# Kernel optimization log

Hardware: AMD Instinct MI355X
Metric: run time of the kernel (lower is better)

## Reference

```python
import jax, jax.numpy as jnp
import numpy as np

N = 50000      # nodes
E = 800000     # edges (before self-loops)
IN = 256       # in_channels
HID = 16       # hidden_channels per head
HEADS = 8
OUT = 64       # out_channels (classes)
NEG_SLOPE = 0.2  # PyG GATConv leaky_relu slope


def setup_inputs() -> dict:
    key = jax.random.key(0)
    ks = jax.random.split(key, 10)
    x = jax.random.normal(ks[0], (N, IN), jnp.float32)
    edge_index = jax.random.randint(ks[1], (2, E), 0, N, dtype=jnp.int32)
    g = lambda k, shape: jax.random.normal(k, shape, jnp.float32) * (1.0 / np.sqrt(shape[0]))
    W1 = g(ks[2], (IN, HEADS * HID))
    a_src1 = jax.random.normal(ks[3], (HEADS, HID), jnp.float32) * 0.1
    a_dst1 = jax.random.normal(ks[4], (HEADS, HID), jnp.float32) * 0.1
    b1 = jnp.zeros((HEADS * HID,), jnp.float32)
    W2 = g(ks[5], (HEADS * HID, OUT))
    a_src2 = jax.random.normal(ks[6], (1, OUT), jnp.float32) * 0.1
    a_dst2 = jax.random.normal(ks[7], (1, OUT), jnp.float32) * 0.1
    b2 = jnp.zeros((OUT,), jnp.float32)
    return {"x": x, "edge_index": edge_index, "W1": W1, "a_src1": a_src1,
            "a_dst1": a_dst1, "b1": b1, "W2": W2, "a_src2": a_src2,
            "a_dst2": a_dst2, "b2": b2}


def gat_conv(x, src, dst, W, a_s, a_d, b, heads, concat):
    # x: [n, f]; edges src->dst; attention softmax over incoming edges of dst
    n = x.shape[0]
    h = (x @ W).reshape(n, heads, -1)                 # [n, H, d]
    al_s = jnp.einsum('nhd,hd->nh', h, a_s)           # [n, H]
    al_d = jnp.einsum('nhd,hd->nh', h, a_d)
    e = jax.nn.leaky_relu(al_s[src] + al_d[dst], negative_slope=NEG_SLOPE)  # [E, H]
    m = jax.ops.segment_max(e, dst, num_segments=n)   # stable scatter-softmax
    ex = jnp.exp(e - m[dst])
    den = jax.ops.segment_sum(ex, dst, num_segments=n)
    alpha = ex / (den[dst] + 1e-16)                   # [E, H]
    out = jax.ops.segment_sum(h[src] * alpha[:, :, None], dst, num_segments=n)  # [n, H, d]
    out = out.reshape(n, -1) if concat else out.mean(axis=1)
    return out + b


def reference(x, edge_index, W1, a_src1, a_dst1, b1, W2, a_src2, a_dst2, b2):
    # inference mode: dropout disabled. PyG GATConv adds self-loops by default.
    n = x.shape[0]
    loop = jnp.arange(n, dtype=edge_index.dtype)
    ei = jnp.concatenate([edge_index, jnp.stack([loop, loop])], axis=1)
    src, dst = ei[0], ei[1]
    h = gat_conv(x, src, dst, W1, a_src1, a_dst1, b1, HEADS, True)
    h = jax.nn.elu(h)
    h = gat_conv(h, src, dst, W2, a_src2, a_dst2, b2, 1, False)
    return jax.nn.log_softmax(h, axis=1)
```

## Files before the change

kernel.cpp:

```cpp
#include <hip/hip_runtime.h>
#include <hip/hip_bf16.h>


typedef __attribute__((ext_vector_type(8))) short short8;
typedef __attribute__((ext_vector_type(4))) float f4;
typedef __attribute__((ext_vector_type(2))) float float2v;

#define NCHUNK 64
#define NRANGE 4
#define RSIZE 16384
#define CONVB 80

#define A1PAD 72
#define B1PAD 264
#define G2PAD 136

__device__ __forceinline__ unsigned short f2bf(float f) {
  unsigned int u = __builtin_bit_cast(unsigned int, f);
  u += 0x7fffu + ((u >> 16) & 1u);
  return (unsigned short)(u >> 16);
}
__device__ __forceinline__ float bf2f(unsigned short h) {
  unsigned int u = ((unsigned int)h) << 16;
  return __builtin_bit_cast(float, u);
}

__device__ __forceinline__ unsigned char f2fp8(float f) {
  unsigned int u = __builtin_bit_cast(unsigned int, f);
  unsigned int s = (u >> 24) & 0x80u;
  float a = fabsf(f);
  a = fminf(a, 448.f);
  if (a < 0.015625f) {
    int m = (int)rintf(a * 512.f);
    return (unsigned char)(s | (unsigned)m);
  }
  unsigned int ub = __builtin_bit_cast(unsigned int, a);
  ub += 0xFFFFFu + ((ub >> 20) & 1u);
  unsigned int e = (ub >> 23) - 120u;
  unsigned int m = (ub >> 20) & 7u;
  if (e > 15u) { e = 15u; m = 6u; }
  return (unsigned char)(s | (e << 3) | m);
}

__global__ __launch_bounds__(512) void hist_kernel(const int* __restrict__ ei,
                                                   int* __restrict__ hist,
                                                   const float* __restrict__ W1,
                                                   const float* __restrict__ W2,
                                                   unsigned short* __restrict__ Wt1,
                                                   unsigned short* __restrict__ Wt2,
                                                   int E, int N, int ET, int CS) {
  if (blockIdx.x >= NCHUNK * NRANGE) {
    int i = (blockIdx.x - NCHUNK * NRANGE) * 512 + threadIdx.x;
    if (i < 128 * 256) {
      int n = i >> 8, k = i & 255;
      Wt1[i] = f2bf(W1[k * 128 + n]);
    } else {
      int j = i - 128 * 256;
      if (j < 64 * 128) {
        int n = j >> 7, k = j & 127;
        Wt2[j] = f2bf(W2[k * 64 + n]);
      }
    }
    return;
  }
  __shared__ int lh[RSIZE];
  const int c = blockIdx.x & (NCHUNK - 1);
  const int r = blockIdx.x >> 6;
  const int base = r * RSIZE;
  for (int i = threadIdx.x; i < RSIZE; i += 512) lh[i] = 0;
  __syncthreads();
  const int e0 = c * CS, e1 = min(e0 + CS, ET);
  for (int e = e0 + threadIdx.x; e < e1; e += 512) {
    int d = (e < E) ? ei[E + e] : (e - E);
    unsigned dl = (unsigned)(d - base);
    if (dl < RSIZE) atomicAdd(&lh[dl], 1);
  }
  __syncthreads();
  for (int i = threadIdx.x; i < RSIZE; i += 512) {
    int d = base + i;
    if (d < N) hist[c * N + d] = lh[i];
  }
}

__global__ __launch_bounds__(256) void colscan_kernel(int* __restrict__ hist,
                                                      int* __restrict__ deg, int N) {
  int d = blockIdx.x * 256 + threadIdx.x;
  if (d >= N) return;
  int run = 0;
#pragma unroll 8
  for (int c = 0; c < NCHUNK; ++c) {
    int v = hist[c * N + d];
    hist[c * N + d] = run;
    run += v;
  }
  deg[d] = run;
}

__global__ __launch_bounds__(1024) void scan1_kernel(const int* __restrict__ deg,
                                                     int* __restrict__ rowptr,
                                                     int* __restrict__ bsum, int N) {
  __shared__ int wtot[16];
  const int lane = threadIdx.x & 63, wid = threadIdx.x >> 6;
  int i = blockIdx.x * 1024 + threadIdx.x;
  int v = (i < N) ? deg[i] : 0;
  int incl = v;
#pragma unroll
  for (int off = 1; off < 64; off <<= 1) {
    int t = __shfl_up(incl, off, 64);
    if (lane >= off) incl += t;
  }
  if (lane == 63) wtot[wid] = incl;
  __syncthreads();
  int woff = 0;
#pragma unroll
  for (int w = 0; w < 16; ++w) woff += (w < wid) ? wtot[w] : 0;
  if (i < N) rowptr[i] = woff + incl - v;
  if (threadIdx.x == 1023) bsum[blockIdx.x] = woff + incl;
}

__global__ __launch_bounds__(256) void scan3_kernel(int* __restrict__ rowptr,
                                                    const int* __restrict__ bsum,
                                                    int N, int ET) {
  int lane = threadIdx.x & 63;
  int g = blockIdx.x >> 2;
  int bv = (lane < g) ? bsum[lane] : 0;
#pragma unroll
  for (int off = 32; off; off >>= 1) bv += __shfl_xor(bv, off, 64);
  int i = blockIdx.x * 256 + threadIdx.x;
  if (i < N) rowptr[i] += bv;
  if (i == N) rowptr[N] = ET;
}

__global__ __launch_bounds__(512) void scatter2_kernel(const int* __restrict__ ei,
                                                       const int* __restrict__ hist,
                                                       const int* __restrict__ rowptr,
                                                       int* __restrict__ csr_src,
                                                       int E, int N, int ET, int CS) {
  __shared__ int lh[RSIZE];
  const int c = blockIdx.x & (NCHUNK - 1);
  const int r = blockIdx.x >> 6;
  const int base = r * RSIZE;
  for (int i = threadIdx.x; i < RSIZE; i += 512) {
    int d = base + i;
    lh[i] = (d < N) ? (rowptr[d] + hist[c * N + d]) : 0;
  }
  __syncthreads();
  const int e0 = c * CS, e1 = min(e0 + CS, ET);
  for (int e = e0 + threadIdx.x; e < e1; e += 512) {
    int s, d;
    if (e < E) { s = ei[e]; d = ei[E + e]; }
    else       { s = e - E; d = s; }
    unsigned dl = (unsigned)(d - base);
    if (dl < RSIZE) {
      int slot = atomicAdd(&lh[dl], 1);
      csr_src[slot] = s;
    }
  }
}

__global__ __launch_bounds__(256) void gemm1_mfma(const float* __restrict__ X,
                                                  const unsigned short* __restrict__ Wt,
                                                  const float* __restrict__ as1,
                                                  const float* __restrict__ ad1,
                                                  unsigned char* __restrict__ H,
                                                  float* __restrict__ als,
                                                  float* __restrict__ ald,
                                                  int M) {
  __shared__ unsigned short Bs[64 * B1PAD];
  __shared__ unsigned short As[2][64 * A1PAD];
  const int t = threadIdx.x;
  const int ln = t & 63;
  const int wv = t >> 6;
  const int ml = ln & 15, q = ln >> 4;
  const int ch = blockIdx.x & 1;
  const int rb = (blockIdx.x >> 1) * 64;
  const int r0 = rb + wv * 16;
  const int alr = wv * 16 + ml;

  int srow[4], skg[4];
#pragma unroll
  for (int i = 0; i < 4; ++i) {
    int g = i * 256 + t;
    srow[i] = g >> 4;
    skg[i] = g & 15;
  }

  float4 astg[4];
#pragma unroll
  for (int i = 0; i < 4; ++i)
    astg[i] = *(const float4*)(X + (size_t)min(rb + srow[i], M - 1) * 256 + skg[i] * 4);

#pragma unroll
  for (int i = 0; i < 8; ++i) {
    int g = i * 256 + t;
    int brow = g >> 5, bc = g & 31;
    *(short8*)&Bs[brow * B1PAD + bc * 8] =
        *(const short8*)(Wt + (size_t)(ch * 64 + brow) * 256 + bc * 8);
  }

#pragma unroll
  for (int i = 0; i < 4; ++i) {
    ushort4 pk;
    pk.x = f2bf(astg[i].x); pk.y = f2bf(astg[i].y);
    pk.z = f2bf(astg[i].z); pk.w = f2bf(astg[i].w);
    *(ushort4*)&As[0][srow[i] * A1PAD + skg[i] * 4] = pk;
  }
  __syncthreads();

  f4 acc[4];
#pragma unroll
  for (int b = 0; b < 4; ++b) acc[b] = (f4)0.f;

#pragma unroll
  for (int s = 0; s < 4; ++s) {
    const int buf = s & 1;
    if (s < 3) {
#pragma unroll
      for (int i = 0; i < 4; ++i)
        astg[i] = *(const float4*)(X + (size_t)min(rb + srow[i], M - 1) * 256 +
                                   (s + 1) * 64 + skg[i] * 4);
    }
#pragma unroll
    for (int kk = 0; kk < 2; ++kk) {
      short8 av = *(const short8*)&As[buf][alr * A1PAD + kk * 32 + q * 8];
#pragma unroll
      for (int b = 0; b < 4; ++b) {
        short8 bfr = *(const short8*)&Bs[(b * 16 + ml) * B1PAD + s * 64 + kk * 32 + q * 8];
        acc[b] = __builtin_amdgcn_mfma_f32_16x16x32_bf16(av, bfr, acc[b], 0, 0, 0);
      }
    }
    if (s < 3) {
#pragma unroll
      for (int i = 0; i < 4; ++i) {
        ushort4 pk;
        pk.x = f2bf(astg[i].x); pk.y = f2bf(astg[i].y);
        pk.z = f2bf(astg[i].z); pk.w = f2bf(astg[i].w);
        *(ushort4*)&As[buf ^ 1][srow[i] * A1PAD + skg[i] * 4] = pk;
      }
    }
    __syncthreads();
  }

#pragma unroll
  for (int i = 0; i < 4; ++i) {
    int rr = r0 + q * 4 + i;
    bool ok = rr < M;
    if (ok) {
#pragma unroll
      for (int b = 0; b < 4; ++b)
        H[(size_t)rr * 128 + ch * 64 + b * 16 + ml] = f2fp8(acc[b][i]);
    }
#pragma unroll
    for (int b = 0; b < 4; ++b) {
      float ps = acc[b][i] * as1[ch * 64 + b * 16 + ml];
      float pd = acc[b][i] * ad1[ch * 64 + b * 16 + ml];
#pragma unroll
      for (int off = 1; off < 16; off <<= 1) {
        ps += __shfl_xor(ps, off, 16);
        pd += __shfl_xor(pd, off, 16);
      }
      if (ok && ml == b) {
        als[(size_t)rr * 8 + ch * 4 + b] = ps;
        ald[(size_t)rr * 8 + ch * 4 + b] = pd;
      }
    }
  }
}

__global__ __launch_bounds__(256) void gemm2_mfma(const unsigned short* __restrict__ Xb,
                                                  const unsigned short* __restrict__ Wt,
                                                  const float* __restrict__ as2,
                                                  const float* __restrict__ ad2,
                                                  unsigned char* __restrict__ H,
                                                  float* __restrict__ als,
                                                  float* __restrict__ ald,
                                                  int M) {
  __shared__ unsigned short Asl[64 * G2PAD];
  __shared__ unsigned short Bsl[64 * G2PAD];
  const int t = threadIdx.x;
  const int ln = t & 63;
  const int wv = t >> 6;
  const int ml = ln & 15, q = ln >> 4;
  const int rb = blockIdx.x * 64;
  const int r0 = rb + wv * 16;
  const int alr = wv * 16 + ml;

#pragma unroll
  for (int i = 0; i < 4; ++i) {
    int g = i * 256 + t;
    int row = g >> 4, kg = g & 15;
    *(short8*)&Asl[row * G2PAD + kg * 8] =
        *(const short8*)(Xb + (size_t)min(rb + row, M - 1) * 128 + kg * 8);
    *(short8*)&Bsl[row * G2PAD + kg * 8] =
        *(const short8*)(Wt + (size_t)row * 128 + kg * 8);
  }
  __syncthreads();

  short8 av[4];
#pragma unroll
  for (int s = 0; s < 4; ++s)
    av[s] = *(const short8*)&Asl[alr * G2PAD + s * 32 + q * 8];

  f4 acc[4];
#pragma unroll
  for (int b = 0; b < 4; ++b) acc[b] = (f4)0.f;

#pragma unroll
  for (int s = 0; s < 4; ++s) {
#pragma unroll
    for (int b = 0; b < 4; ++b) {
      short8 bfr = *(const short8*)&Bsl[(b * 16 + ml) * G2PAD + s * 32 + q * 8];
      acc[b] = __builtin_amdgcn_mfma_f32_16x16x32_bf16(av[s], bfr, acc[b], 0, 0, 0);
    }
  }

#pragma unroll
  for (int i = 0; i < 4; ++i) {
    int rr = r0 + q * 4 + i;
    bool ok = rr < M;
    if (ok) {
#pragma unroll
      for (int b = 0; b < 4; ++b)
        H[(size_t)rr * 64 + b * 16 + ml] = f2fp8(acc[b][i]);
    }
    float ps = 0.f, pd = 0.f;
#pragma unroll
    for (int b = 0; b < 4; ++b) {
      ps += acc[b][i] * as2[b * 16 + ml];
      pd += acc[b][i] * ad2[b * 16 + ml];
    }
#pragma unroll
    for (int off = 1; off < 16; off <<= 1) {
      ps += __shfl_xor(ps, off, 16);
      pd += __shfl_xor(pd, off, 16);
    }
    if (ok && ml == 0) { als[rr] = ps; ald[rr] = pd; }
  }
}

__global__ __launch_bounds__(256) void attn1_kernel(
    const unsigned char* __restrict__ h1, const float* __restrict__ als,
    const float* __restrict__ ald, const float* __restrict__ b1,
    const int* __restrict__ rowptr, const int* __restrict__ csr_src,
    unsigned short* __restrict__ helu, int N) {
  int d = __builtin_amdgcn_readfirstlane(
      (blockIdx.x * blockDim.x + threadIdx.x) >> 6);
  int lane = threadIdx.x & 63;
  if (d >= N) return;
  const int hh = lane >> 3;
  const int hw = lane & 7;
  const int ew = lane >> 3;
  const float aldp = ald[d * 8 + hw];
  const int beg = rowptr[d], end = rowptr[d + 1];
  const unsigned char* h1l = h1 + 2 * lane;
  float den = 0.f, ax = 0.f, ay = 0.f;

  int idx0 = beg + ew;
  int se = csr_src[idx0 < end ? idx0 : end - 1];
  for (int p0 = beg; p0 < end; p0 += 8) {
    int p1 = p0 + 8;
    int se_n = se;
    if (p1 < end) {
      int idx1 = p1 + ew;
      se_n = csr_src[idx1 < end ? idx1 : end - 1];
    }
    float v = als[se * 8 + hw] + aldp;
    v = fmaxf(v, 0.2f * v);
    float w = ((p0 + ew) < end) ? __expf(v) : 0.f;
    int sjv[8];
#pragma unroll
    for (int j = 0; j < 8; ++j) sjv[j] = __shfl(se, j * 8);
    unsigned short pkv[8];
#pragma unroll
    for (int j = 0; j < 8; ++j)
      pkv[j] = *(const unsigned short*)(h1l + (size_t)sjv[j] * 128);
#pragma unroll
    for (int j = 0; j < 8; ++j) {
      float wj = __shfl(w, j * 8 + hh);
      float2v g = __builtin_amdgcn_cvt_pk_f32_fp8(pkv[j], false);
      den += wj; ax += wj * g.x; ay += wj * g.y;
    }
    se = se_n;
  }

  float inv = 1.0f / (den + 1e-16f);
  float2 bb = *(const float2*)(b1 + 2 * lane);
  float o0 = ax * inv + bb.x;
  float o1 = ay * inv + bb.y;
  o0 = o0 > 0.f ? o0 : __expf(o0) - 1.0f;
  o1 = o1 > 0.f ? o1 : __expf(o1) - 1.0f;
  ushort2 ov; ov.x = f2bf(o0); ov.y = f2bf(o1);
  *(ushort2*)(helu + (size_t)d * 128 + 2 * lane) = ov;
}

__global__ __launch_bounds__(256) void attn2_kernel(
    const unsigned char* __restrict__ h2, const float* __restrict__ als,
    const float* __restrict__ ald, const float* __restrict__ b2,
    const int* __restrict__ rowptr, const int* __restrict__ csr_src,
    float* __restrict__ out, int N) {
  int d = __builtin_amdgcn_readfirstlane(
      (blockIdx.x * blockDim.x + threadIdx.x) >> 6);
  int lane = threadIdx.x & 63;
  if (d >= N) return;
  const float aldd = ald[d];
  const int beg = rowptr[d], end = rowptr[d + 1];
  const unsigned char* h2l = h2 + lane;
  float den = 0.f, acc = 0.f;

  int idx0 = beg + lane;
  int se = csr_src[idx0 < end ? idx0 : end - 1];
  for (int p0 = beg; p0 < end; p0 += 64) {
    int p1 = p0 + 64;
    int se_n = se;
    if (p1 < end) {
      int i1 = p1 + lane;
      se_n = csr_src[i1 < end ? i1 : end - 1];
    }
    float v = als[se] + aldd;
    v = fmaxf(v, 0.2f * v);
    float w = ((p0 + lane) < end) ? __expf(v) : 0.f;
    int cnt = min(64, end - p0);
    for (int j0 = 0; j0 < cnt; j0 += 8) {
      int sjv[8];
#pragma unroll
      for (int j = 0; j < 8; ++j) sjv[j] = __shfl(se, j0 + j);
      float gv[8];
#pragma unroll
      for (int j = 0; j < 8; ++j)
        gv[j] = __builtin_amdgcn_cvt_f32_fp8(h2l[(size_t)sjv[j] * 64], 0);
#pragma unroll
      for (int j = 0; j < 8; ++j) {
        float wj = __shfl(w, j0 + j);
        den += wj; acc += wj * gv[j];
      }
    }
    se = se_n;
  }

  float z = acc / (den + 1e-16f) + b2[lane];
  float zm = z;
#pragma unroll
  for (int off = 32; off; off >>= 1) zm = fmaxf(zm, __shfl_xor(zm, off, 64));
  float ex = __expf(z - zm), se2 = ex;
#pragma unroll
  for (int off = 32; off; off >>= 1) se2 += __shfl_xor(se2, off, 64);
  out[(size_t)d * 64 + lane] = z - zm - __logf(se2);
}

extern "C" void kernel_launch(void* const* d_in, const int* in_sizes, int n_in,
                              void* d_out, int out_size, void* d_ws, size_t ws_size,
                              hipStream_t stream) {
  const int N = in_sizes[0] / 256;
  const int E = in_sizes[1] / 2;
  const int ET = E + N;
  const int CS = (ET + NCHUNK - 1) / NCHUNK;
  const int NB = (N + 1023) / 1024;

  const float* x   = (const float*)d_in[0];
  const int*   ei  = (const int*)d_in[1];
  const float* W1  = (const float*)d_in[2];
  const float* as1 = (const float*)d_in[3];
  const float* ad1 = (const float*)d_in[4];
  const float* b1  = (const float*)d_in[5];
  const float* W2  = (const float*)d_in[6];
  const float* as2 = (const float*)d_in[7];
  const float* ad2 = (const float*)d_in[8];
  const float* b2  = (const float*)d_in[9];
  float* out = (float*)d_out;

  char* p = (char*)d_ws;
  unsigned char* h1f8 = (unsigned char*)p; p += (size_t)N * 128;
  unsigned char* h2f8 = h1f8;
  unsigned short* helu = (unsigned short*)p; p += (size_t)NCHUNK * N * 4;
  int* hist = (int*)helu;
  unsigned short* Wt1  = (unsigned short*)p; p += (size_t)128 * 256 * 2;
  unsigned short* Wt2  = (unsigned short*)p; p += (size_t)64 * 128 * 2;
  float* als1 = (float*)p; p += (size_t)N * 8 * 4;
  float* ald1 = (float*)p; p += (size_t)N * 8 * 4;
  float* als2 = (float*)p; p += (size_t)N * 4;
  float* ald2 = (float*)p; p += (size_t)N * 4;
  int* deg     = (int*)p; p += (size_t)N * 4;
  int* rowptr  = (int*)p; p += (size_t)(N + 1) * 4;
  int* bsum    = (int*)p; p += 64 * 4;
  int* csr_src = (int*)p; p += (size_t)ET * 4;

  hist_kernel<<<NCHUNK * NRANGE + CONVB, 512, 0, stream>>>(ei, hist, W1, W2, Wt1, Wt2,
                                                           E, N, ET, CS);
  colscan_kernel<<<(N + 255) / 256, 256, 0, stream>>>(hist, deg, N);
  scan1_kernel<<<NB, 1024, 0, stream>>>(deg, rowptr, bsum, N);
  scan3_kernel<<<(N + 256) / 256, 256, 0, stream>>>(rowptr, bsum, N, ET);
  scatter2_kernel<<<NCHUNK * NRANGE, 512, 0, stream>>>(ei, hist, rowptr, csr_src, E, N, ET, CS);

  gemm1_mfma<<<2 * ((N + 63) / 64), 256, 0, stream>>>(x, Wt1, as1, ad1, h1f8, als1, ald1, N);
  attn1_kernel<<<(N + 3) / 4, 256, 0, stream>>>(h1f8, als1, ald1, b1, rowptr, csr_src, helu, N);

  gemm2_mfma<<<(N + 63) / 64, 256, 0, stream>>>(helu, Wt2, as2, ad2, h2f8, als2, ald2, N);
  attn2_kernel<<<(N + 3) / 4, 256, 0, stream>>>(h2f8, als2, ald2, b2, rowptr, csr_src, out, N);
}
```

Baseline: 247.6 us.

## Vectorize attention gathers with 16-byte loads and cross-lane reductions

Both attention kernels are remapped so each lane loads a 16-byte chunk of an fp8 source row and accumulates 16 features. Several edges are handled in parallel across lane groups, and partial sums are combined at the end with xor-shuffle reductions. The first layer uses 8 lanes per edge (one per head); the second uses 4 lanes per edge with 16 edges per step. This replaces many narrow per-lane byte and short gathers, plus the per-edge broadcast shuffles, with fewer wide loads. The cost is more registers and a reduction tail of many shuffles per node, which matters at low average degree.

Measured after the change: 282.5 us. +14.1%, slower.

```diff
diff --git a/kernel.cpp b/kernel.cpp
--- a/kernel.cpp
+++ b/kernel.cpp
@@ -347,50 +347,66 @@
       (blockIdx.x * blockDim.x + threadIdx.x) >> 6);
   int lane = threadIdx.x & 63;
   if (d >= N) return;
-  const int hh = lane >> 3;
-  const int hw = lane & 7;
-  const int ew = lane >> 3;
-  const float aldp = ald[d * 8 + hw];
+  const int g = lane >> 3;
+  const int f = lane & 7;
+  const float aldp = ald[d * 8 + f];
   const int beg = rowptr[d], end = rowptr[d + 1];
-  const unsigned char* h1l = h1 + 2 * lane;
-  float den = 0.f, ax = 0.f, ay = 0.f;
-
-  int idx0 = beg + ew;
+  float den = 0.f;
+  float acc[16];
+#pragma unroll
+  for (int k = 0; k < 16; ++k) acc[k] = 0.f;
+
+  int idx0 = beg + g;
   int se = csr_src[idx0 < end ? idx0 : end - 1];
   for (int p0 = beg; p0 < end; p0 += 8) {
     int p1 = p0 + 8;
     int se_n = se;
     if (p1 < end) {
-      int idx1 = p1 + ew;
-      se_n = csr_src[idx1 < end ? idx1 : end - 1];
-    }
-    float v = als[se * 8 + hw] + aldp;
+      int i1 = p1 + g;
+      se_n = csr_src[i1 < end ? i1 : end - 1];
+    }
+    float v = als[se * 8 + f] + aldp;
     v = fmaxf(v, 0.2f * v);
-    float w = ((p0 + ew) < end) ? __expf(v) : 0.f;
-    int sjv[8];
-#pragma unroll
-    for (int j = 0; j < 8; ++j) sjv[j] = __shfl(se, j * 8);
-    unsigned short pkv[8];
-#pragma unroll
-    for (int j = 0; j < 8; ++j)
-      pkv[j] = *(const unsigned short*)(h1l + (size_t)sjv[j] * 128);
+    float w = ((p0 + g) < end) ? __expf(v) : 0.f;
+    short8 hv = *(const short8*)(h1 + (size_t)se * 128 + f * 16);
+    den += w;
 #pragma unroll
     for (int j = 0; j < 8; ++j) {
-      float wj = __shfl(w, j * 8 + hh);
-      float2v g = __builtin_amdgcn_cvt_pk_f32_fp8(pkv[j], false);
-      den += wj; ax += wj * g.x; ay += wj * g.y;
+      float2v u = __builtin_amdgcn_cvt_pk_f32_fp8((unsigned short)hv[j], false);
+      acc[2 * j]     += w * u.x;
+      acc[2 * j + 1] += w * u.y;
     }
     se = se_n;
   }
 
+#pragma unroll
+  for (int off = 8; off < 64; off <<= 1) {
+    den += __shfl_xor(den, off, 64);
+#pragma unroll
+    for (int k = 0; k < 16; ++k) acc[k] += __shfl_xor(acc[k], off, 64);
+  }
+
   float inv = 1.0f / (den + 1e-16f);
-  float2 bb = *(const float2*)(b1 + 2 * lane);
-  float o0 = ax * inv + bb.x;
-  float o1 = ay * inv + bb.y;
-  o0 = o0 > 0.f ? o0 : __expf(o0) - 1.0f;
-  o1 = o1 > 0.f ? o1 : __expf(o1) - 1.0f;
-  ushort2 ov; ov.x = f2bf(o0); ov.y = f2bf(o1);
-  *(ushort2*)(helu + (size_t)d * 128 + 2 * lane) = ov;
+  const float4* bv = (const float4*)(b1 + f * 16);
+  float o[16];
+#pragma unroll
+  for (int qq = 0; qq < 4; ++qq) {
+    float4 bb = bv[qq];
+    o[qq * 4 + 0] = acc[qq * 4 + 0] * inv + bb.x;
+    o[qq * 4 + 1] = acc[qq * 4 + 1] * inv + bb.y;
+    o[qq * 4 + 2] = acc[qq * 4 + 2] * inv + bb.z;
+    o[qq * 4 + 3] = acc[qq * 4 + 3] * inv + bb.w;
+  }
+#pragma unroll
+  for (int k = 0; k < 16; ++k)
+    o[k] = o[k] > 0.f ? o[k] : __expf(o[k]) - 1.0f;
+
+  if (g < 2) {
+    short8 ov;
+#pragma unroll
+    for (int j = 0; j < 8; ++j) ov[j] = (short)f2bf(o[g * 8 + j]);
+    *(short8*)(helu + (size_t)d * 128 + f * 16 + g * 8) = ov;
+  }
 }
 
 __global__ __launch_bounds__(256) void attn2_kernel(
@@ -402,10 +418,14 @@
       (blockIdx.x * blockDim.x + threadIdx.x) >> 6);
   int lane = threadIdx.x & 63;
   if (d >= N) return;
+  const int g = lane >> 2;
+  const int c = lane & 3;
   const float aldd = ald[d];
   const int beg = rowptr[d], end = rowptr[d + 1];
-  const unsigned char* h2l = h2 + lane;
-  float den = 0.f, acc = 0.f;
+  float den = 0.f;
+  float acc[16];
+#pragma unroll
+  for (int k = 0; k < 16; ++k) acc[k] = 0.f;
 
   int idx0 = beg + lane;
   int se = csr_src[idx0 < end ? idx0 : end - 1];
@@ -420,31 +440,59 @@
     v = fmaxf(v, 0.2f * v);
     float w = ((p0 + lane) < end) ? __expf(v) : 0.f;
     int cnt = min(64, end - p0);
-    for (int j0 = 0; j0 < cnt; j0 += 8) {
-      int sjv[8];
-#pragma unroll
-      for (int j = 0; j < 8; ++j) sjv[j] = __shfl(se, j0 + j);
-      float gv[8];
-#pragma unroll
-      for (int j = 0; j < 8; ++j)
-        gv[j] = __builtin_amdgcn_cvt_f32_fp8(h2l[(size_t)sjv[j] * 64], 0);
+    for (int j0 = 0; j0 < cnt; j0 += 16) {
+      int se16 = __shfl(se, j0 + g);
+      float w16 = __shfl(w, j0 + g);
+      short8 hv = *(const short8*)(h2 + (size_t)se16 * 64 + c * 16);
+      den += w16;
 #pragma unroll
       for (int j = 0; j < 8; ++j) {
-        float wj = __shfl(w, j0 + j);
-        den += wj; acc += wj * gv[j];
+        float2v u = __builtin_amdgcn_cvt_pk_f32_fp8((unsigned short)hv[j], false);
+        acc[2 * j]     += w16 * u.x;
+        acc[2 * j + 1] += w16 * u.y;
       }
     }
     se = se_n;
   }
 
-  float z = acc / (den + 1e-16f) + b2[lane];
-  float zm = z;
-#pragma unroll
-  for (int off = 32; off; off >>= 1) zm = fmaxf(zm, __shfl_xor(zm, off, 64));
-  float ex = __expf(z - zm), se2 = ex;
-#pragma unroll
-  for (int off = 32; off; off >>= 1) se2 += __shfl_xor(se2, off, 64);
-  out[(size_t)d * 64 + lane] = z - zm - __logf(se2);
+#pragma unroll
+  for (int off = 4; off < 64; off <<= 1) {
+    den += __shfl_xor(den, off, 64);
+#pragma unroll
+    for (int k = 0; k < 16; ++k) acc[k] += __shfl_xor(acc[k], off, 64);
+  }
+
+  float inv = 1.0f / (den + 1e-16f);
+  const float4* bv = (const float4*)(b2 + c * 16);
+  float z[16];
+#pragma unroll
+  for (int qq = 0; qq < 4; ++qq) {
+    float4 bb = bv[qq];
+    z[qq * 4 + 0] = acc[qq * 4 + 0] * inv + bb.x;
+    z[qq * 4 + 1] = acc[qq * 4 + 1] * inv + bb.y;
+    z[qq * 4 + 2] = acc[qq * 4 + 2] * inv + bb.z;
+    z[qq * 4 + 3] = acc[qq * 4 + 3] * inv + bb.w;
+  }
+  float zm = z[0];
+#pragma unroll
+  for (int k = 1; k < 16; ++k) zm = fmaxf(zm, z[k]);
+  zm = fmaxf(zm, __shfl_xor(zm, 1, 64));
+  zm = fmaxf(zm, __shfl_xor(zm, 2, 64));
+  float se2 = 0.f;
+#pragma unroll
+  for (int k = 0; k < 16; ++k) se2 += __expf(z[k] - zm);
+  se2 += __shfl_xor(se2, 1, 64);
+  se2 += __shfl_xor(se2, 2, 64);
+  float lse = __logf(se2);
+
+  if (lane < 16) {
+    float4 ov;
+    ov.x = z[g * 4 + 0] - zm - lse;
+    ov.y = z[g * 4 + 1] - zm - lse;
+    ov.z = z[g * 4 + 2] - zm - lse;
+    ov.w = z[g * 4 + 3] - zm - lse;
+    *(float4*)(out + (size_t)d * 64 + c * 16 + g * 4) = ov;
+  }
 }
 
 extern "C" void kernel_launch(void* const* d_in, const int* in_sizes, int n_in,
```

## Fuse CSR scatter and layer-1 GEMM into one launch with block-range dispatch

Applied to the files above, without the earlier changes.

The CSR scatter kernel and the first MFMA GEMM are merged into a single kernel, with the first 512 blocks doing the scatter and the rest doing the GEMM. The two independent stages can then run concurrently on the GPU instead of back to back, and one launch gap goes away. The scatter is re-tiled to 8 ranges of 8192 destinations with 256 threads, so its LDS histogram fits in the GEMM's shared buffer. It also loads the source index only for edges that fall in the block's range. In exchange, scatter blocks now reserve the larger GEMM LDS allocation, which may reduce occupancy, and each edge chunk is read by twice as many blocks.

Result: slower. 253.6 us (+2.4%).

```diff
diff --git a/kernel.cpp b/kernel.cpp
--- a/kernel.cpp
+++ b/kernel.cpp
@@ -10,6 +10,9 @@
 #define NRANGE 4
 #define RSIZE 16384
 #define CONVB 80
+
+#define SC_NRANGE 8
+#define SC_RSIZE 8192
 
 #define A1PAD 72
 #define B1PAD 264
@@ -131,49 +134,49 @@
   if (i == N) rowptr[N] = ET;
 }
 
-__global__ __launch_bounds__(512) void scatter2_kernel(const int* __restrict__ ei,
-                                                       const int* __restrict__ hist,
-                                                       const int* __restrict__ rowptr,
-                                                       int* __restrict__ csr_src,
-                                                       int E, int N, int ET, int CS) {
-  __shared__ int lh[RSIZE];
-  const int c = blockIdx.x & (NCHUNK - 1);
-  const int r = blockIdx.x >> 6;
-  const int base = r * RSIZE;
-  for (int i = threadIdx.x; i < RSIZE; i += 512) {
-    int d = base + i;
-    lh[i] = (d < N) ? (rowptr[d] + hist[c * N + d]) : 0;
-  }
-  __syncthreads();
-  const int e0 = c * CS, e1 = min(e0 + CS, ET);
-  for (int e = e0 + threadIdx.x; e < e1; e += 512) {
-    int s, d;
-    if (e < E) { s = ei[e]; d = ei[E + e]; }
-    else       { s = e - E; d = s; }
-    unsigned dl = (unsigned)(d - base);
-    if (dl < RSIZE) {
-      int slot = atomicAdd(&lh[dl], 1);
-      csr_src[slot] = s;
-    }
-  }
-}
-
-__global__ __launch_bounds__(256) void gemm1_mfma(const float* __restrict__ X,
-                                                  const unsigned short* __restrict__ Wt,
-                                                  const float* __restrict__ as1,
-                                                  const float* __restrict__ ad1,
-                                                  unsigned char* __restrict__ H,
-                                                  float* __restrict__ als,
-                                                  float* __restrict__ ald,
-                                                  int M) {
-  __shared__ unsigned short Bs[64 * B1PAD];
-  __shared__ unsigned short As[2][64 * A1PAD];
+__global__ __launch_bounds__(256) void sg1_kernel(
+    const int* __restrict__ ei, const int* __restrict__ hist,
+    const int* __restrict__ rowptr, int* __restrict__ csr_src,
+    const float* __restrict__ X, const unsigned short* __restrict__ Wt,
+    const float* __restrict__ as1, const float* __restrict__ ad1,
+    unsigned char* __restrict__ H, float* __restrict__ als,
+    float* __restrict__ ald,
+    int E, int N, int ET, int CS, int M) {
+  __shared__ __align__(16) char smem[64 * B1PAD * 2 + 2 * 64 * A1PAD * 2];
+
+  if (blockIdx.x < NCHUNK * SC_NRANGE) {
+    int* lh = (int*)smem;
+    const int c = blockIdx.x & (NCHUNK - 1);
+    const int r = blockIdx.x >> 6;
+    const int base = r * SC_RSIZE;
+    for (int i = threadIdx.x; i < SC_RSIZE; i += 256) {
+      int d = base + i;
+      lh[i] = (d < N) ? (rowptr[d] + hist[c * N + d]) : 0;
+    }
+    __syncthreads();
+    const int e0 = c * CS, e1 = min(e0 + CS, ET);
+    for (int e = e0 + threadIdx.x; e < e1; e += 256) {
+      int d = (e < E) ? ei[E + e] : (e - E);
+      unsigned dl = (unsigned)(d - base);
+      if (dl < SC_RSIZE) {
+        int s = (e < E) ? ei[e] : (e - E);
+        int slot = atomicAdd(&lh[dl], 1);
+        csr_src[slot] = s;
+      }
+    }
+    return;
+  }
+
+  unsigned short* Bs = (unsigned short*)smem;
+  unsigned short (*As)[64 * A1PAD] =
+      (unsigned short (*)[64 * A1PAD])(smem + 64 * B1PAD * 2);
+  const int bb = blockIdx.x - NCHUNK * SC_NRANGE;
   const int t = threadIdx.x;
   const int ln = t & 63;
   const int wv = t >> 6;
   const int ml = ln & 15, q = ln >> 4;
-  const int ch = blockIdx.x & 1;
-  const int rb = (blockIdx.x >> 1) * 64;
+  const int ch = bb & 1;
+  const int rb = (bb >> 1) * 64;
   const int r0 = rb + wv * 16;
   const int alr = wv * 16 + ml;
 
@@ -455,6 +458,7 @@
   const int ET = E + N;
   const int CS = (ET + NCHUNK - 1) / NCHUNK;
   const int NB = (N + 1023) / 1024;
+  const int G1 = 2 * ((N + 63) / 64);
 
   const float* x   = (const float*)d_in[0];
   const int*   ei  = (const int*)d_in[1];
@@ -489,9 +493,11 @@
   colscan_kernel<<<(N + 255) / 256, 256, 0, stream>>>(hist, deg, N);
   scan1_kernel<<<NB, 1024, 0, stream>>>(deg, rowptr, bsum, N);
   scan3_kernel<<<(N + 256) / 256, 256, 0, stream>>>(rowptr, bsum, N, ET);
-  scatter2_kernel<<<NCHUNK * NRANGE, 512, 0, stream>>>(ei, hist, rowptr, csr_src, E, N, ET, CS);
-
-  gemm1_mfma<<<2 * ((N + 63) / 64), 256, 0, stream>>>(x, Wt1, as1, ad1, h1f8, als1, ald1, N);
+
+  sg1_kernel<<<NCHUNK * SC_NRANGE + G1, 256, 0, stream>>>(
+      ei, hist, rowptr, csr_src, x, Wt1, as1, ad1, h1f8, als1, ald1,
+      E, N, ET, CS, N);
+
   attn1_kernel<<<(N + 3) / 4, 256, 0, stream>>>(h1f8, als1, ald1, b1, rowptr, csr_src, helu, N);
 
   gemm2_mfma<<<(N + 63) / 64, 256, 0, stream>>>(helu, Wt2, as2, ad2, h2f8, als2, ald2, N);
```

## Load full K-slab of X and W into k-major LDS once in gemm1

Applied to the files above, without the earlier changes.

Replaces gemm1's double-buffered, padded row-major LDS staging with a single up-front load of the whole 64x256 A tile and 64x256 B tile into a k-segment-major shared-memory layout. The MFMA loop then runs over 8 k-steps with no intermediate barriers. This removes the per-stage syncs and is meant to make LDS fragment reads conflict-free without padding. In exchange all global loads sit in registers at once, raising register pressure, and there is no longer overlap of loads with MFMA inside the block.

New measurement: 250.5 us. About the same (+1.1%).

```diff
diff --git a/kernel.cpp b/kernel.cpp
--- a/kernel.cpp
+++ b/kernel.cpp
@@ -11,8 +11,6 @@
 #define RSIZE 16384
 #define CONVB 80
 
-#define A1PAD 72
-#define B1PAD 264
 #define G2PAD 136
 
 __device__ __forceinline__ unsigned short f2bf(float f) {
@@ -166,8 +164,8 @@
                                                   float* __restrict__ als,
                                                   float* __restrict__ ald,
                                                   int M) {
-  __shared__ unsigned short Bs[64 * B1PAD];
-  __shared__ unsigned short As[2][64 * A1PAD];
+  __shared__ unsigned short A2[64 * 256];
+  __shared__ unsigned short B2[64 * 256];
   const int t = threadIdx.x;
   const int ln = t & 63;
   const int wv = t >> 6;
@@ -177,33 +175,30 @@
   const int r0 = rb + wv * 16;
   const int alr = wv * 16 + ml;
 
-  int srow[4], skg[4];
-#pragma unroll
-  for (int i = 0; i < 4; ++i) {
-    int g = i * 256 + t;
-    srow[i] = g >> 4;
-    skg[i] = g & 15;
-  }
-
-  float4 astg[4];
-#pragma unroll
-  for (int i = 0; i < 4; ++i)
-    astg[i] = *(const float4*)(X + (size_t)min(rb + srow[i], M - 1) * 256 + skg[i] * 4);
-
-#pragma unroll
-  for (int i = 0; i < 8; ++i) {
-    int g = i * 256 + t;
-    int brow = g >> 5, bc = g & 31;
-    *(short8*)&Bs[brow * B1PAD + bc * 8] =
-        *(const short8*)(Wt + (size_t)(ch * 64 + brow) * 256 + bc * 8);
-  }
-
-#pragma unroll
-  for (int i = 0; i < 4; ++i) {
-    ushort4 pk;
-    pk.x = f2bf(astg[i].x); pk.y = f2bf(astg[i].y);
-    pk.z = f2bf(astg[i].z); pk.w = f2bf(astg[i].w);
-    *(ushort4*)&As[0][srow[i] * A1PAD + skg[i] * 4] = pk;
+  const int srow = t >> 2;
+  const int klo  = t & 3;
+
+  const float* xp = X + (size_t)min(rb + srow, M - 1) * 256;
+  const unsigned short* wp = Wt + (size_t)(ch * 64 + srow) * 256;
+  float4 xa[8][2];
+  short8 wb[8];
+#pragma unroll
+  for (int it = 0; it < 8; ++it) {
+    int kseg = it * 4 + klo;
+    xa[it][0] = *(const float4*)(xp + kseg * 8);
+    xa[it][1] = *(const float4*)(xp + kseg * 8 + 4);
+    wb[it]    = *(const short8*)(wp + kseg * 8);
+  }
+#pragma unroll
+  for (int it = 0; it < 8; ++it) {
+    int kseg = it * 4 + klo;
+    short8 av;
+    av[0] = (short)f2bf(xa[it][0].x); av[1] = (short)f2bf(xa[it][0].y);
+    av[2] = (short)f2bf(xa[it][0].z); av[3] = (short)f2bf(xa[it][0].w);
+    av[4] = (short)f2bf(xa[it][1].x); av[5] = (short)f2bf(xa[it][1].y);
+    av[6] = (short)f2bf(xa[it][1].z); av[7] = (short)f2bf(xa[it][1].w);
+    *(short8*)&A2[(kseg * 64 + srow) * 8] = av;
+    *(short8*)&B2[(kseg * 64 + srow) * 8] = wb[it];
   }
   __syncthreads();
 
@@ -212,33 +207,14 @@
   for (int b = 0; b < 4; ++b) acc[b] = (f4)0.f;
 
 #pragma unroll
-  for (int s = 0; s < 4; ++s) {
-    const int buf = s & 1;
-    if (s < 3) {
-#pragma unroll
-      for (int i = 0; i < 4; ++i)
-        astg[i] = *(const float4*)(X + (size_t)min(rb + srow[i], M - 1) * 256 +
-                                   (s + 1) * 64 + skg[i] * 4);
-    }
-#pragma unroll
-    for (int kk = 0; kk < 2; ++kk) {
-      short8 av = *(const short8*)&As[buf][alr * A1PAD + kk * 32 + q * 8];
-#pragma unroll
-      for (int b = 0; b < 4; ++b) {
-        short8 bfr = *(const short8*)&Bs[(b * 16 + ml) * B1PAD + s * 64 + kk * 32 + q * 8];
-        acc[b] = __builtin_amdgcn_mfma_f32_16x16x32_bf16(av, bfr, acc[b], 0, 0, 0);
-      }
-    }
-    if (s < 3) {
-#pragma unroll
-      for (int i = 0; i < 4; ++i) {
-        ushort4 pk;
-        pk.x = f2bf(astg[i].x); pk.y = f2bf(astg[i].y);
-        pk.z = f2bf(astg[i].z); pk.w = f2bf(astg[i].w);
-        *(ushort4*)&As[buf ^ 1][srow[i] * A1PAD + skg[i] * 4] = pk;
-      }
-    }
-    __syncthreads();
+  for (int s = 0; s < 8; ++s) {
+    const int kc = s * 4 + q;
+    short8 av = *(const short8*)&A2[(kc * 64 + alr) * 8];
+#pragma unroll
+    for (int b = 0; b < 4; ++b) {
+      short8 bfr = *(const short8*)&B2[(kc * 64 + b * 16 + ml) * 8];
+      acc[b] = __builtin_amdgcn_mfma_f32_16x16x32_bf16(av, bfr, acc[b], 0, 0, 0);
+    }
   }
 
 #pragma unroll
```
